# Performance work log

Hardware: AMD Instinct MI355X
Metric: run time of the kernel (lower is better)

The kernel has to match this reference:

```python
import jax, jax.numpy as jnp
import numpy as np

N_NODES = 50000
N_EDGES = 800000
D_IN = 128
D_OUT = 64


def setup_inputs() -> dict:
    key = jax.random.key(0)
    k1, k2, k3, k4, k5 = jax.random.split(key, 5)
    x = jax.random.normal(k1, (N_NODES, D_IN), dtype=jnp.float32)
    edge_src = jax.random.randint(k2, (N_EDGES,), 0, N_NODES, dtype=jnp.int32)
    edge_dst = jax.random.randint(k3, (N_EDGES,), 0, N_NODES, dtype=jnp.int32)
    edge_vals = jax.random.uniform(k4, (N_EDGES,), dtype=jnp.float32)
    # xavier_normal init for weight, zeros for bias (matches torch init)
    std = float(np.sqrt(2.0 / (D_IN + D_OUT)))
    W = jax.random.normal(k5, (D_IN, D_OUT), dtype=jnp.float32) * std
    b = jnp.zeros((D_OUT,), dtype=jnp.float32)
    return {"x": x, "edge_src": edge_src, "edge_dst": edge_dst,
            "edge_vals": edge_vals, "W": W, "b": b}


def reference(x, edge_src, edge_dst, edge_vals, W, b):
    # support = x @ W  : dense feature transform [N, D_OUT]
    support = jnp.dot(x, W)
    # sparse adj @ support via gather + weighted segment-sum over edges
    # adj[dst, src] = edge_vals  ->  out[dst] = sum_e vals[e] * support[src[e]]
    msgs = support[edge_src] * edge_vals[:, None]  # [E, D_OUT]
    out = jax.ops.segment_sum(msgs, edge_dst, num_segments=N_NODES)
    out = out + b
    return jax.nn.relu(out)
```

## Files before the change

kernel.cpp:

```cpp
#include <hip/hip_runtime.h>

#define N_NODES 50000
#define N_EDGES_MAX 800000
#define D_IN    128
#define D_OUT   64

#define BW      64
#define BSHIFT  6
#define NBKT    ((N_NODES + BW - 1) / BW)
#define BPAD    1024
#define PCHUNK  4096
#define HCHUNK  8192
#define ACH     2048

#define NPB 16

__global__ __launch_bounds__(256) void gemm_xw(
    const float* __restrict__ x, const float* __restrict__ W,
    float* __restrict__ support) {
  __shared__ float Wlds[D_IN][D_OUT];
  __shared__ float xlds[NPB][D_IN];
  const int tid = threadIdx.x;
  const int node0 = blockIdx.x * NPB;

  const float4* W4 = (const float4*)W;
  float4* Wl4 = (float4*)Wlds;
#pragma unroll
  for (int i = 0; i < (D_IN * D_OUT / 4) / 256; ++i)
    Wl4[tid + i * 256] = W4[tid + i * 256];

  const float4* x4 = (const float4*)(x + (size_t)node0 * D_IN);
  float4* xl4 = (float4*)xlds;
#pragma unroll
  for (int i = 0; i < (NPB * D_IN / 4) / 256; ++i)
    xl4[tid + i * 256] = x4[tid + i * 256];

  __syncthreads();

  const int f = tid & 63;
  const int g = tid >> 6;
  float acc0 = 0.f, acc1 = 0.f, acc2 = 0.f, acc3 = 0.f;

#pragma unroll
  for (int k = 0; k < D_IN; k += 4) {
    const float w0 = Wlds[k + 0][f];
    const float w1 = Wlds[k + 1][f];
    const float w2 = Wlds[k + 2][f];
    const float w3 = Wlds[k + 3][f];
    const float4 xa = *(const float4*)&xlds[g * 4 + 0][k];
    const float4 xb = *(const float4*)&xlds[g * 4 + 1][k];
    const float4 xc = *(const float4*)&xlds[g * 4 + 2][k];
    const float4 xd = *(const float4*)&xlds[g * 4 + 3][k];
    acc0 += xa.x * w0 + xa.y * w1 + xa.z * w2 + xa.w * w3;
    acc1 += xb.x * w0 + xb.y * w1 + xb.z * w2 + xb.w * w3;
    acc2 += xc.x * w0 + xc.y * w1 + xc.z * w2 + xc.w * w3;
    acc3 += xd.x * w0 + xd.y * w1 + xd.z * w2 + xd.w * w3;
  }

  const int nbase = node0 + g * 4;
  support[(size_t)(nbase + 0) * D_OUT + f] = acc0;
  support[(size_t)(nbase + 1) * D_OUT + f] = acc1;
  support[(size_t)(nbase + 2) * D_OUT + f] = acc2;
  support[(size_t)(nbase + 3) * D_OUT + f] = acc3;
}

__global__ __launch_bounds__(256) void hist_bucket(
    const int* __restrict__ edst, int* __restrict__ gcnt, int n_edges) {
  __shared__ int lh[BPAD];
  const int t = threadIdx.x;
  for (int b = t; b < BPAD; b += 256) lh[b] = 0;
  __syncthreads();
  const int e0 = blockIdx.x * HCHUNK;
  const int e1 = min(e0 + HCHUNK, n_edges);
  for (int i = e0 + t; i < e1; i += 256)
    atomicAdd(&lh[edst[i] >> BSHIFT], 1);
  __syncthreads();
  for (int b = t; b < BPAD; b += 256) {
    const int c = lh[b];
    if (c) atomicAdd(&gcnt[b], c);
  }
}

__global__ __launch_bounds__(1024) void scan_bucket(
    const int* __restrict__ gcnt, int* __restrict__ goff,
    int* __restrict__ gcur) {
  __shared__ int s[BPAD];
  const int t = threadIdx.x;
  const int c = gcnt[t];
  s[t] = c;
  __syncthreads();
  for (int off = 1; off < BPAD; off <<= 1) {
    const int o = (t >= off) ? s[t - off] : 0;
    __syncthreads();
    s[t] += o;
    __syncthreads();
  }
  const int ex = s[t] - c;
  goff[t] = ex;
  gcur[t] = ex;
}

__global__ __launch_bounds__(512) void partition(
    const int* __restrict__ esrc, const int* __restrict__ edst,
    const float* __restrict__ eval, int* __restrict__ gcur,
    int2* __restrict__ svp, int n_edges) {
  __shared__ int lh[BPAD], lscan[BPAD], lcur[BPAD], lbase[BPAD];
  __shared__ int tsum[512];
  __shared__ int2 stage[PCHUNK];
  const int t = threadIdx.x;
  const int e0 = blockIdx.x * PCHUNK;
  const int e1 = min(e0 + PCHUNK, n_edges);

  lh[t] = 0; lh[t + 512] = 0;
  __syncthreads();

  int  rs[8], rd[8];
  float rv[8];
#pragma unroll
  for (int k = 0; k < 8; ++k) {
    const int i = e0 + t + k * 512;
    if (i < e1) {
      rs[k] = esrc[i]; rd[k] = edst[i]; rv[k] = eval[i];
      atomicAdd(&lh[rd[k] >> BSHIFT], 1);
    } else {
      rs[k] = -1; rd[k] = 0; rv[k] = 0.f;
    }
  }
  __syncthreads();

  const int a  = lh[2 * t];
  const int b2 = lh[2 * t + 1];
  tsum[t] = a + b2;
  __syncthreads();
  for (int off = 1; off < 512; off <<= 1) {
    const int o = (t >= off) ? tsum[t - off] : 0;
    __syncthreads();
    tsum[t] += o;
    __syncthreads();
  }
  const int ex = tsum[t] - (a + b2);
  lscan[2 * t]     = ex;
  lscan[2 * t + 1] = ex + a;
  lcur[2 * t]      = ex;
  lcur[2 * t + 1]  = ex + a;
  if (a)  lbase[2 * t]     = atomicAdd(&gcur[2 * t], a);
  if (b2) lbase[2 * t + 1] = atomicAdd(&gcur[2 * t + 1], b2);
  __syncthreads();

#pragma unroll
  for (int k = 0; k < 8; ++k) {
    if (rs[k] >= 0) {
      const int b = rd[k] >> BSHIFT;
      const int r = atomicAdd(&lcur[b], 1);
      stage[r] = make_int2((rs[k] & 0xFFFF) | ((rd[k] & (BW - 1)) << 16),
                           __float_as_int(rv[k]));
    }
  }
  __syncthreads();

  const int kn = e1 - e0;
  for (int p = t; p < kn; p += 512) {
    int lo = 0, hi = BPAD - 1;
    while (lo < hi) {
      const int mid = (lo + hi + 1) >> 1;
      if (lscan[mid] <= p) lo = mid; else hi = mid - 1;
    }
    svp[lbase[lo] + (p - lscan[lo])] = stage[p];
  }
}

__global__ __launch_bounds__(512) void aggregate_bucket(
    const float* __restrict__ support, const int* __restrict__ goff,
    const int2* __restrict__ svp, const float* __restrict__ bias,
    float* __restrict__ out) {
  __shared__ int2 sorted[ACH];
  __shared__ int h[BW];
  __shared__ int ro[BW + 1];
  __shared__ int cur[BW];
  const int t = threadIdx.x;
  const int f = t & 63;
  const int wid = t >> 6;
  const int bkt = blockIdx.x;
  const int beg = goff[bkt];
  const int end = goff[bkt + 1];

  float acc[8];
#pragma unroll
  for (int k = 0; k < 8; ++k) acc[k] = 0.f;

  for (int cbeg = beg; cbeg < end; cbeg += ACH) {
    const int cn = min(ACH, end - cbeg);
    if (t < BW) h[t] = 0;
    __syncthreads();

    int2 m0 = make_int2(0, 0), m1 = m0, m2 = m0, m3 = m0;
    const int i0 = t, i1 = t + 512, i2 = t + 1024, i3 = t + 1536;
    if (i0 < cn) { m0 = svp[cbeg + i0]; atomicAdd(&h[m0.x >> 16], 1); }
    if (i1 < cn) { m1 = svp[cbeg + i1]; atomicAdd(&h[m1.x >> 16], 1); }
    if (i2 < cn) { m2 = svp[cbeg + i2]; atomicAdd(&h[m2.x >> 16], 1); }
    if (i3 < cn) { m3 = svp[cbeg + i3]; atomicAdd(&h[m3.x >> 16], 1); }
    __syncthreads();

    if (wid == 0) {
      const int c = h[f];
      int v = c;
#pragma unroll
      for (int off = 1; off < 64; off <<= 1) {
        const int u = __shfl_up(v, off);
        if (f >= off) v += u;
      }
      const int exo = v - c;
      ro[f] = exo;
      cur[f] = exo;
      if (f == 63) ro[64] = cn;
    }
    __syncthreads();

    if (i0 < cn) { const int r = atomicAdd(&cur[m0.x >> 16], 1); sorted[r] = m0; }
    if (i1 < cn) { const int r = atomicAdd(&cur[m1.x >> 16], 1); sorted[r] = m1; }
    if (i2 < cn) { const int r = atomicAdd(&cur[m2.x >> 16], 1); sorted[r] = m2; }
    if (i3 < cn) { const int r = atomicAdd(&cur[m3.x >> 16], 1); sorted[r] = m3; }
    __syncthreads();

#pragma unroll
    for (int k = 0; k < 8; ++k) {
      const int row = wid * 8 + k;
      const int rb = ro[row];
      const int re = ro[row + 1];
      for (int j = rb; j < re; ++j) {
        const int2 e = sorted[j];
        acc[k] += support[(size_t)(e.x & 0xFFFF) * D_OUT + f] *
                  __int_as_float(e.y);
      }
    }
    __syncthreads();
  }

  const float bf = bias[f];
  const int nbase = bkt * BW;
#pragma unroll
  for (int k = 0; k < 8; ++k) {
    const int node = nbase + wid * 8 + k;
    if (node < N_NODES)
      out[(size_t)node * D_OUT + f] = fmaxf(acc[k] + bf, 0.f);
  }
}

#define EPG 8
__global__ __launch_bounds__(256) void scatter_edges(
    const float* __restrict__ support, const int* __restrict__ esrc,
    const int* __restrict__ edst, const float* __restrict__ eval,
    float* __restrict__ out, int n_edges) {
  const int tid = threadIdx.x;
  const int f = tid & 63;
  const int grp = blockIdx.x * 4 + (tid >> 6);
  const int e0 = grp * EPG;
  int s[EPG], d[EPG];
  float v[EPG];
#pragma unroll
  for (int i = 0; i < EPG; ++i) {
    const int e = e0 + i;
    if (e < n_edges) { s[i] = esrc[e]; d[i] = edst[e]; v[i] = eval[e]; }
    else             { s[i] = 0; d[i] = 0; v[i] = 0.f; }
  }
  float m[EPG];
#pragma unroll
  for (int i = 0; i < EPG; ++i)
    m[i] = support[(size_t)s[i] * D_OUT + f] * v[i];
#pragma unroll
  for (int i = 0; i < EPG; ++i)
    if (e0 + i < n_edges) atomicAdd(&out[(size_t)d[i] * D_OUT + f], m[i]);
}

__global__ __launch_bounds__(256) void bias_relu(
    float* __restrict__ out, const float* __restrict__ b) {
  const int i = blockIdx.x * 256 + threadIdx.x;
  float4* o4 = (float4*)out;
  float4 v = o4[i];
  const int fb = (i * 4) & 63;
  const float4 bb = *(const float4*)&b[fb];
  v.x = fmaxf(v.x + bb.x, 0.f);
  v.y = fmaxf(v.y + bb.y, 0.f);
  v.z = fmaxf(v.z + bb.z, 0.f);
  v.w = fmaxf(v.w + bb.w, 0.f);
  o4[i] = v;
}

extern "C" void kernel_launch(void* const* d_in, const int* in_sizes, int n_in,
                              void* d_out, int out_size, void* d_ws, size_t ws_size,
                              hipStream_t stream) {
  const float* x    = (const float*)d_in[0];
  const int*   esrc = (const int*)  d_in[1];
  const int*   edst = (const int*)  d_in[2];
  const float* eval = (const float*)d_in[3];
  const float* W    = (const float*)d_in[4];
  const float* b    = (const float*)d_in[5];
  float* out = (float*)d_out;
  const int n_edges = in_sizes[1];

  size_t off = 0;
  auto alloc = [&](size_t bytes) {
    size_t o = off;
    off = (off + bytes + 255) & ~(size_t)255;
    return o;
  };
  char* ws = (char*)d_ws;
  const size_t sup_o  = alloc((size_t)N_NODES * D_OUT * sizeof(float));
  const size_t cnt_o  = alloc((size_t)BPAD * sizeof(int));
  const size_t offs_o = alloc((size_t)BPAD * sizeof(int));
  const size_t cur_o  = alloc((size_t)BPAD * sizeof(int));
  const size_t svp_o  = alloc((size_t)N_EDGES_MAX * sizeof(int2));
  const size_t req = off;

  float* support = (float*)(ws + sup_o);

  gemm_xw<<<N_NODES / NPB, 256, 0, stream>>>(x, W, support);

  if (ws_size >= req && n_edges <= N_EDGES_MAX) {
    int*  gcnt = (int*) (ws + cnt_o);
    int*  goff = (int*) (ws + offs_o);
    int*  gcur = (int*) (ws + cur_o);
    int2* svp  = (int2*)(ws + svp_o);

    hipMemsetAsync(gcnt, 0, (size_t)BPAD * sizeof(int), stream);

    hist_bucket<<<(n_edges + HCHUNK - 1) / HCHUNK, 256, 0, stream>>>(
        edst, gcnt, n_edges);
    scan_bucket<<<1, BPAD, 0, stream>>>(gcnt, goff, gcur);
    partition<<<(n_edges + PCHUNK - 1) / PCHUNK, 512, 0, stream>>>(
        esrc, edst, eval, gcur, svp, n_edges);
    aggregate_bucket<<<NBKT, 512, 0, stream>>>(support, goff, svp, b, out);
  } else {
    hipMemsetAsync(d_out, 0, (size_t)N_NODES * D_OUT * sizeof(float), stream);
    const int groups = (n_edges + EPG - 1) / EPG;
    scatter_edges<<<(groups + 3) / 4, 256, 0, stream>>>(support, esrc, edst,
                                                        eval, out, n_edges);
    bias_relu<<<N_NODES * D_OUT / 4 / 256, 256, 0, stream>>>(out, b);
  }
}
```

Baseline: 197.8 us.

## Use wave-shuffle scans, embed bucket id in staging, interleave aggregate row loops

Replaces the LDS Hillis-Steele scans in scan_bucket and partition with wavefront shuffle scans plus a small per-wave prefix, removing many barriers. Partition stores the bucket index in the staged word so the scatter-out no longer binary-searches the local scan. Aggregate drops to 256 threads per block, each wave owning 16 rows and advancing them round-robin so several independent gathers are in flight. HCHUNK is halved. The interleaved loop increases register use and branching, and with fewer threads the bucket-local sort and load take more steps per thread.

```diff
diff --git a/kernel.cpp b/kernel.cpp
--- a/kernel.cpp
+++ b/kernel.cpp
@@ -10,7 +10,7 @@
 #define NBKT    ((N_NODES + BW - 1) / BW)
 #define BPAD    1024
 #define PCHUNK  4096
-#define HCHUNK  8192
+#define HCHUNK  4096
 #define ACH     2048
 
 #define NPB 16
@@ -81,23 +81,32 @@
   }
 }
 
-__global__ __launch_bounds__(1024) void scan_bucket(
+__global__ __launch_bounds__(256) void scan_bucket(
     const int* __restrict__ gcnt, int* __restrict__ goff,
     int* __restrict__ gcur) {
-  __shared__ int s[BPAD];
-  const int t = threadIdx.x;
-  const int c = gcnt[t];
-  s[t] = c;
-  __syncthreads();
-  for (int off = 1; off < BPAD; off <<= 1) {
-    const int o = (t >= off) ? s[t - off] : 0;
-    __syncthreads();
-    s[t] += o;
-    __syncthreads();
-  }
-  const int ex = s[t] - c;
-  goff[t] = ex;
-  gcur[t] = ex;
+  __shared__ int wsum[4], wpre[4];
+  const int t = threadIdx.x, lane = t & 63, w = t >> 6;
+  const int4 c = *(const int4*)(gcnt + 4 * t);
+  const int s = c.x + c.y + c.z + c.w;
+  int incl = s;
+#pragma unroll
+  for (int off = 1; off < 64; off <<= 1) {
+    const int u = __shfl_up(incl, off);
+    if (lane >= off) incl += u;
+  }
+  if (lane == 63) wsum[w] = incl;
+  __syncthreads();
+  if (t == 0) {
+    int run = 0;
+#pragma unroll
+    for (int i = 0; i < 4; ++i) { wpre[i] = run; run += wsum[i]; }
+  }
+  __syncthreads();
+  const int ex = wpre[w] + incl - s;
+  int4 o;
+  o.x = ex; o.y = ex + c.x; o.z = ex + c.x + c.y; o.w = ex + c.x + c.y + c.z;
+  *(int4*)(goff + 4 * t) = o;
+  *(int4*)(gcur + 4 * t) = o;
 }
 
 __global__ __launch_bounds__(512) void partition(
@@ -105,9 +114,10 @@
     const float* __restrict__ eval, int* __restrict__ gcur,
     int2* __restrict__ svp, int n_edges) {
   __shared__ int lh[BPAD], lscan[BPAD], lcur[BPAD], lbase[BPAD];
-  __shared__ int tsum[512];
+  __shared__ int wsum[8], wpre[8];
   __shared__ int2 stage[PCHUNK];
   const int t = threadIdx.x;
+  const int lane = t & 63, w = t >> 6;
   const int e0 = blockIdx.x * PCHUNK;
   const int e1 = min(e0 + PCHUNK, n_edges);
 
@@ -130,15 +140,22 @@
 
   const int a  = lh[2 * t];
   const int b2 = lh[2 * t + 1];
-  tsum[t] = a + b2;
-  __syncthreads();
-  for (int off = 1; off < 512; off <<= 1) {
-    const int o = (t >= off) ? tsum[t - off] : 0;
-    __syncthreads();
-    tsum[t] += o;
-    __syncthreads();
-  }
-  const int ex = tsum[t] - (a + b2);
+  const int s = a + b2;
+  int incl = s;
+#pragma unroll
+  for (int off = 1; off < 64; off <<= 1) {
+    const int u = __shfl_up(incl, off);
+    if (lane >= off) incl += u;
+  }
+  if (lane == 63) wsum[w] = incl;
+  __syncthreads();
+  if (t == 0) {
+    int run = 0;
+#pragma unroll
+    for (int i = 0; i < 8; ++i) { wpre[i] = run; run += wsum[i]; }
+  }
+  __syncthreads();
+  const int ex = wpre[w] + incl - s;
   lscan[2 * t]     = ex;
   lscan[2 * t + 1] = ex + a;
   lcur[2 * t]      = ex;
@@ -152,7 +169,7 @@
     if (rs[k] >= 0) {
       const int b = rd[k] >> BSHIFT;
       const int r = atomicAdd(&lcur[b], 1);
-      stage[r] = make_int2((rs[k] & 0xFFFF) | ((rd[k] & (BW - 1)) << 16),
+      stage[r] = make_int2(rs[k] | ((rd[k] & (BW - 1)) << 16) | (b << 22),
                            __float_as_int(rv[k]));
     }
   }
@@ -160,16 +177,13 @@
 
   const int kn = e1 - e0;
   for (int p = t; p < kn; p += 512) {
-    int lo = 0, hi = BPAD - 1;
-    while (lo < hi) {
-      const int mid = (lo + hi + 1) >> 1;
-      if (lscan[mid] <= p) lo = mid; else hi = mid - 1;
-    }
-    svp[lbase[lo] + (p - lscan[lo])] = stage[p];
-  }
-}
-
-__global__ __launch_bounds__(512) void aggregate_bucket(
+    const int2 e = stage[p];
+    const int b = (int)((unsigned)e.x >> 22);
+    svp[lbase[b] + (p - lscan[b])] = make_int2(e.x & 0x3FFFFF, e.y);
+  }
+}
+
+__global__ __launch_bounds__(256) void aggregate_bucket(
     const float* __restrict__ support, const int* __restrict__ goff,
     const int2* __restrict__ svp, const float* __restrict__ bias,
     float* __restrict__ out) {
@@ -184,21 +198,26 @@
   const int beg = goff[bkt];
   const int end = goff[bkt + 1];
 
-  float acc[8];
-#pragma unroll
-  for (int k = 0; k < 8; ++k) acc[k] = 0.f;
+  float acc[16];
+#pragma unroll
+  for (int k = 0; k < 16; ++k) acc[k] = 0.f;
 
   for (int cbeg = beg; cbeg < end; cbeg += ACH) {
     const int cn = min(ACH, end - cbeg);
     if (t < BW) h[t] = 0;
     __syncthreads();
 
-    int2 m0 = make_int2(0, 0), m1 = m0, m2 = m0, m3 = m0;
-    const int i0 = t, i1 = t + 512, i2 = t + 1024, i3 = t + 1536;
-    if (i0 < cn) { m0 = svp[cbeg + i0]; atomicAdd(&h[m0.x >> 16], 1); }
-    if (i1 < cn) { m1 = svp[cbeg + i1]; atomicAdd(&h[m1.x >> 16], 1); }
-    if (i2 < cn) { m2 = svp[cbeg + i2]; atomicAdd(&h[m2.x >> 16], 1); }
-    if (i3 < cn) { m3 = svp[cbeg + i3]; atomicAdd(&h[m3.x >> 16], 1); }
+    int2 m[8];
+#pragma unroll
+    for (int k = 0; k < 8; ++k) {
+      const int i = t + k * 256;
+      if (i < cn) {
+        m[k] = svp[cbeg + i];
+        atomicAdd(&h[(m[k].x >> 16) & 63], 1);
+      } else {
+        m[k] = make_int2(-1, 0);
+      }
+    }
     __syncthreads();
 
     if (wid == 0) {
@@ -209,28 +228,38 @@
         const int u = __shfl_up(v, off);
         if (f >= off) v += u;
       }
-      const int exo = v - c;
-      ro[f] = exo;
-      cur[f] = exo;
+      ro[f] = v - c;
+      cur[f] = v - c;
       if (f == 63) ro[64] = cn;
     }
     __syncthreads();
 
-    if (i0 < cn) { const int r = atomicAdd(&cur[m0.x >> 16], 1); sorted[r] = m0; }
-    if (i1 < cn) { const int r = atomicAdd(&cur[m1.x >> 16], 1); sorted[r] = m1; }
-    if (i2 < cn) { const int r = atomicAdd(&cur[m2.x >> 16], 1); sorted[r] = m2; }
-    if (i3 < cn) { const int r = atomicAdd(&cur[m3.x >> 16], 1); sorted[r] = m3; }
-    __syncthreads();
-
 #pragma unroll
     for (int k = 0; k < 8; ++k) {
-      const int row = wid * 8 + k;
-      const int rb = ro[row];
-      const int re = ro[row + 1];
-      for (int j = rb; j < re; ++j) {
-        const int2 e = sorted[j];
-        acc[k] += support[(size_t)(e.x & 0xFFFF) * D_OUT + f] *
-                  __int_as_float(e.y);
+      if (m[k].x >= 0) {
+        const int r = atomicAdd(&cur[(m[k].x >> 16) & 63], 1);
+        sorted[r] = m[k];
+      }
+    }
+    __syncthreads();
+
+    int idx[16], iend[16];
+#pragma unroll
+    for (int k = 0; k < 16; ++k) {
+      idx[k]  = ro[wid * 16 + k];
+      iend[k] = ro[wid * 16 + k + 1];
+    }
+    bool active = true;
+    while (active) {
+      active = false;
+#pragma unroll
+      for (int k = 0; k < 16; ++k) {
+        if (idx[k] < iend[k]) {
+          const int2 e = sorted[idx[k]++];
+          acc[k] += support[(size_t)(e.x & 0xFFFF) * D_OUT + f] *
+                    __int_as_float(e.y);
+          active = true;
+        }
       }
     }
     __syncthreads();
@@ -239,8 +268,8 @@
   const float bf = bias[f];
   const int nbase = bkt * BW;
 #pragma unroll
-  for (int k = 0; k < 8; ++k) {
-    const int node = nbase + wid * 8 + k;
+  for (int k = 0; k < 16; ++k) {
+    const int node = nbase + wid * 16 + k;
     if (node < N_NODES)
       out[(size_t)node * D_OUT + f] = fmaxf(acc[k] + bf, 0.f);
   }
@@ -326,10 +355,10 @@
 
     hist_bucket<<<(n_edges + HCHUNK - 1) / HCHUNK, 256, 0, stream>>>(
         edst, gcnt, n_edges);
-    scan_bucket<<<1, BPAD, 0, stream>>>(gcnt, goff, gcur);
+    scan_bucket<<<1, 256, 0, stream>>>(gcnt, goff, gcur);
     partition<<<(n_edges + PCHUNK - 1) / PCHUNK, 512, 0, stream>>>(
         esrc, edst, eval, gcur, svp, n_edges);
-    aggregate_bucket<<<NBKT, 512, 0, stream>>>(support, goff, svp, b, out);
+    aggregate_bucket<<<NBKT, 256, 0, stream>>>(support, goff, svp, b, out);
   } else {
     hipMemsetAsync(d_out, 0, (size_t)N_NODES * D_OUT * sizeof(float), stream);
     const int groups = (n_edges + EPG - 1) / EPG;
```

Result: slower. 231.8 us (+17.2%).
